# Kernel optimization log

Measured on AMD Instinct MI355X. Metric: run time of the kernel, lower is better.

The kernel has to match this reference:

```python
import jax, jax.numpy as jnp
import numpy as np

WINDOW_SIZES = (1, 2, 3)
COV_DIM = 128
MEM_DIM = 128
BATCH = 8192


def setup_inputs() -> dict:
    rng = np.random.default_rng(0)
    sizes = rng.integers(16, 64, size=BATCH)
    total = int(sizes.sum())  # ~327k tokens
    key = jax.random.key(0)
    ks = jax.random.split(key, 10)
    s = 0.05
    inp = {
        "x": jax.random.normal(ks[0], (total, COV_DIM), jnp.float32),
        "sizes": jnp.asarray(sizes, jnp.int32),
    }
    for i, w in enumerate(WINDOW_SIZES):
        inp[f"conv_w{i}"] = jax.random.normal(ks[1 + 2 * i], (MEM_DIM, COV_DIM, w), jnp.float32) * s
        inp[f"conv_b{i}"] = jax.random.normal(ks[2 + 2 * i], (MEM_DIM,), jnp.float32) * s
    inp["lin_w"] = jax.random.normal(ks[7], (MEM_DIM, len(WINDOW_SIZES) * MEM_DIM), jnp.float32) * s
    inp["lin_b"] = jax.random.normal(ks[8], (MEM_DIM,), jnp.float32) * s
    return inp


def _temporal_conv(x, w, b):
    # x: [T, C], w: [M, C, k] -> [T-k+1, M]  (valid 1D conv, as nn.Conv1d)
    y = jax.lax.conv_general_dilated(
        x.T[None],  # [1, C, T]
        w,
        window_strides=(1,),
        padding="VALID",
        dimension_numbers=("NCH", "OIH", "NCH"),
    )[0]  # [M, L]
    return y.T + b


def _dmax(h, sizes, window_size, batch):
    # Ragged per-segment max over dim 0 of the concatenated conv output.
    # Segment i covers rows [off_i, off_i + sizes[i] - window_size + 1) where
    # off_i is the exclusive cumsum of sizes (DMax advances start_idx by sizes[i]).
    L = h.shape[0]  # total - window_size + 1
    cum = jnp.cumsum(sizes)  # [B], inclusive
    p = jnp.arange(L)
    seg = jnp.searchsorted(cum, p, side="right")  # segment owning row p
    valid = p + (window_size - 1) < cum[seg]  # within sizes[i]-w+1 prefix
    seg = jnp.where(valid, seg, batch)  # dump invalid rows in a trash segment
    return jax.ops.segment_max(h, seg, num_segments=batch + 1)[:batch]


def reference(x, sizes, conv_w0, conv_b0, conv_w1, conv_b1, conv_w2, conv_b2, lin_w, lin_b):
    batch = sizes.shape[0]
    convs = ((conv_w0, conv_b0), (conv_w1, conv_b1), (conv_w2, conv_b2))
    pools = []
    for wsz, (cw, cb) in zip(WINDOW_SIZES, convs):
        h = jax.nn.relu(_temporal_conv(x, cw, cb))  # [T-w+1, M]
        pools.append(_dmax(h, sizes, wsz, batch))  # [B, M]
    concat = jnp.concatenate(pools, axis=1)  # [B, 3M]
    return jnp.tanh(concat @ lin_w.T + lin_b)  # [B, M]
```

## Files before the change

kernel.cpp:

```cpp
#include <hip/hip_runtime.h>
#include <hip/hip_bf16.h>

typedef __bf16 bf16x8 __attribute__((ext_vector_type(8)));
typedef __bf16 bf16x4 __attribute__((ext_vector_type(4)));
typedef float  f32x4  __attribute__((ext_vector_type(4)));

#define MFMA16(a, b, c) __builtin_amdgcn_mfma_f32_16x16x32_bf16((a), (b), (c), 0, 0, 0)

__global__ void k_prep(const int* __restrict__ sizes, int* __restrict__ offsets,
                       const float* __restrict__ w0, const float* __restrict__ w1,
                       const float* __restrict__ w2, const float* __restrict__ lw,
                       __bf16* __restrict__ Wpack,
                       __bf16* __restrict__ Lhi, __bf16* __restrict__ Llo) {
  const int bid = blockIdx.x, t = threadIdx.x;
  if (bid == 240) {
    __shared__ int part[256];
    const int base = t * 32;
    int v[32];
    int s = 0;
#pragma unroll
    for (int i = 0; i < 32; ++i) { v[i] = sizes[base + i]; s += v[i]; }
    part[t] = s;
    __syncthreads();
    for (int d = 1; d < 256; d <<= 1) {
      int add = (t >= d) ? part[t - d] : 0;
      __syncthreads();
      part[t] += add;
      __syncthreads();
    }
    int run = (t == 0) ? 0 : part[t - 1];
#pragma unroll
    for (int i = 0; i < 32; ++i) { offsets[base + i] = run; run += v[i]; }
  } else if (bid < 48) {
    const int nt = bid, sl = nt >> 3, f = nt & 7;
    const int kt = t >> 6, lane = t & 63;
    const float* src; int kw, jj;
    if      (sl == 0) { src = w0; kw = 1; jj = 0; }
    else if (sl == 1) { src = w1; kw = 2; jj = 0; }
    else if (sl == 2) { src = w1; kw = 2; jj = 1; }
    else if (sl == 3) { src = w2; kw = 3; jj = 0; }
    else if (sl == 4) { src = w2; kw = 3; jj = 1; }
    else              { src = w2; kw = 3; jj = 2; }
    const int feat  = f * 16 + (lane & 15);
    const int cbase = kt * 32 + ((lane >> 4) << 3);
    __bf16* dst = Wpack + ((((nt * 4 + kt) << 6) + lane) << 3);
#pragma unroll
    for (int j = 0; j < 8; ++j)
      dst[j] = (__bf16)src[(feat * 128 + cbase + j) * kw + jj];
  } else {
    const int idx = (bid - 48) * 256 + t;
    const int j = idx & 7, lane = (idx >> 3) & 63, rest = idx >> 9;
    const int kt = rest % 12, nt = rest / 12;
    const int o = nt * 16 + (lane & 15);
    const int q = kt * 32 + ((lane >> 4) << 3) + j;
    const float v = lw[o * 384 + q];
    const __bf16 hi = (__bf16)v;
    Lhi[idx] = hi;
    Llo[idx] = (__bf16)(v - (float)hi);
  }
}

__global__ __launch_bounds__(256, 4)
void k_conv(const float* __restrict__ x, const int* __restrict__ sizes,
            const int* __restrict__ offsets,
            const float* __restrict__ cb0, const float* __restrict__ cb1,
            const float* __restrict__ cb2,
            const bf16x8* __restrict__ Wpack,
            __bf16* __restrict__ Phi, __bf16* __restrict__ Plo) {
  __shared__ __bf16 xh[66 * 136];
  const int b = blockIdx.x;
  const int s = sizes[b];
  const long off = offsets[b];
  const int t = threadIdx.x;
  const int MT = (s + 15) >> 4;

  {
    const int quads = s << 5;
    float4 v[8];
#pragma unroll
    for (int i = 0; i < 8; ++i) {
      const int qi = t + (i << 8);
      if (qi < quads) {
        const int r = qi >> 5, c = (qi & 31) << 2;
        v[i] = *(const float4*)(x + (off + r) * 128 + c);
      }
    }
#pragma unroll
    for (int i = 0; i < 8; ++i) {
      const int qi = t + (i << 8);
      if (qi < quads) {
        const int r = qi >> 5, c = (qi & 31) << 2;
        bf16x4 h; h[0] = (__bf16)v[i].x; h[1] = (__bf16)v[i].y;
                  h[2] = (__bf16)v[i].z; h[3] = (__bf16)v[i].w;
        *(bf16x4*)&xh[r * 136 + c] = h;
      }
    }
    const int zend = MT * 16 + 2;
    const int c = (t & 31) << 2;
    for (int r = s + (t >> 5); r < zend; r += 8)
      *(bf16x4*)&xh[r * 136 + c] =
          bf16x4{(__bf16)0.f, (__bf16)0.f, (__bf16)0.f, (__bf16)0.f};
  }
  __syncthreads();

  const int wid = t >> 6, lane = t & 63;
  const int lo16 = lane & 15, g16 = lane >> 4;

#pragma unroll
  for (int fi = 0; fi < 2; ++fi) {
    const int ft = wid + (fi << 2);
    const int feat = ft * 16 + lo16;

    f32x4 acc[4][3];
#pragma unroll
    for (int mt = 0; mt < 4; ++mt)
#pragma unroll
      for (int p = 0; p < 3; ++p)
        acc[mt][p] = f32x4{0.f, 0.f, 0.f, 0.f};

#pragma unroll
    for (int kt = 0; kt < 4; ++kt) {
      bf16x8 bf[6];
#pragma unroll
      for (int sl = 0; sl < 6; ++sl)
        bf[sl] = Wpack[(((sl * 8 + ft) * 4 + kt) << 6) + lane];
#pragma unroll
      for (int mt = 0; mt < 4; ++mt) {
        if (mt < MT) {
          const __bf16* ap = &xh[(mt * 16 + lo16) * 136 + kt * 32 + (g16 << 3)];
          const bf16x8 A0 = *(const bf16x8*)ap;
          const bf16x8 A1 = *(const bf16x8*)(ap + 136);
          const bf16x8 A2 = *(const bf16x8*)(ap + 272);
          acc[mt][0] = MFMA16(A0, bf[0], acc[mt][0]);
          acc[mt][1] = MFMA16(A0, bf[1], acc[mt][1]);
          acc[mt][1] = MFMA16(A1, bf[2], acc[mt][1]);
          acc[mt][2] = MFMA16(A0, bf[3], acc[mt][2]);
          acc[mt][2] = MFMA16(A1, bf[4], acc[mt][2]);
          acc[mt][2] = MFMA16(A2, bf[5], acc[mt][2]);
        }
      }
    }

    float m1 = -1e30f, m2 = -1e30f, m3 = -1e30f;
#pragma unroll
    for (int mt = 0; mt < 4; ++mt) {
      if (mt >= MT) continue;
#pragma unroll
      for (int v = 0; v < 4; ++v) {
        const int lrow = mt * 16 + g16 * 4 + v;
        if (lrow < s)     m1 = fmaxf(m1, acc[mt][0][v]);
        if (lrow < s - 1) m2 = fmaxf(m2, acc[mt][1][v]);
        if (lrow < s - 2) m3 = fmaxf(m3, acc[mt][2][v]);
      }
    }
    m1 = fmaxf(m1, __shfl_xor(m1, 16)); m1 = fmaxf(m1, __shfl_xor(m1, 32));
    m2 = fmaxf(m2, __shfl_xor(m2, 16)); m2 = fmaxf(m2, __shfl_xor(m2, 32));
    m3 = fmaxf(m3, __shfl_xor(m3, 16)); m3 = fmaxf(m3, __shfl_xor(m3, 32));
    if (g16 == 0) {
      const float p1 = fmaxf(m1 + cb0[feat], 0.f);
      const float p2 = fmaxf(m2 + cb1[feat], 0.f);
      const float p3 = fmaxf(m3 + cb2[feat], 0.f);
      const __bf16 h1 = (__bf16)p1, h2 = (__bf16)p2, h3 = (__bf16)p3;
      const long row = (long)b * 384;
      Phi[row + feat]       = h1;
      Plo[row + feat]       = (__bf16)(p1 - (float)h1);
      Phi[row + 128 + feat] = h2;
      Plo[row + 128 + feat] = (__bf16)(p2 - (float)h2);
      Phi[row + 256 + feat] = h3;
      Plo[row + 256 + feat] = (__bf16)(p3 - (float)h3);
    }
  }
}

__global__ __launch_bounds__(256, 4)
void k_lin(const __bf16* __restrict__ Phi, const __bf16* __restrict__ Plo,
           const bf16x8* __restrict__ Lhi, const bf16x8* __restrict__ Llo,
           const float* __restrict__ lb, float* __restrict__ out) {
  __shared__ __bf16 ph[16 * 392];
  __shared__ __bf16 pl[16 * 392];
  const int blk = blockIdx.x, t = threadIdx.x;
  const long rbase = (long)blk * 16;
#pragma unroll
  for (int i = 0; i < 3; ++i) {
    const int ci = t + (i << 8);
    const int r = ci / 48, cc = ci % 48;
    *(int4*)&ph[r * 392 + (cc << 3)] = *(const int4*)&Phi[(rbase + r) * 384 + (cc << 3)];
    *(int4*)&pl[r * 392 + (cc << 3)] = *(const int4*)&Plo[(rbase + r) * 384 + (cc << 3)];
  }
  __syncthreads();
  const int wid = t >> 6, lane = t & 63;
  const int lo16 = lane & 15, g = lane >> 4;
#pragma unroll
  for (int ni = 0; ni < 2; ++ni) {
    const int nt = wid + (ni << 2);
    f32x4 acc = f32x4{0.f, 0.f, 0.f, 0.f};
#pragma unroll
    for (int kt = 0; kt < 12; ++kt) {
      const bf16x8 bh = Lhi[((nt * 12 + kt) << 6) + lane];
      const bf16x8 bl = Llo[((nt * 12 + kt) << 6) + lane];
      const int aoff = lo16 * 392 + kt * 32 + (g << 3);
      const bf16x8 ah = *(const bf16x8*)&ph[aoff];
      const bf16x8 al = *(const bf16x8*)&pl[aoff];
      acc = MFMA16(ah, bh, acc);
      acc = MFMA16(al, bh, acc);
      acc = MFMA16(ah, bl, acc);
    }
    const int o = nt * 16 + lo16;
    const float bias = lb[o];
#pragma unroll
    for (int v = 0; v < 4; ++v) {
      const int r = g * 4 + v;
      const float val = acc[v] + bias;
      out[(rbase + r) * 128 + o] = 1.f - 2.f / (__expf(2.f * val) + 1.f);
    }
  }
}

extern "C" void kernel_launch(void* const* d_in, const int* in_sizes, int n_in,
                              void* d_out, int out_size, void* d_ws, size_t ws_size,
                              hipStream_t stream) {
  const float* x   = (const float*)d_in[0];
  const int* sizes = (const int*)d_in[1];
  const float* w0  = (const float*)d_in[2];
  const float* cb0 = (const float*)d_in[3];
  const float* w1  = (const float*)d_in[4];
  const float* cb1 = (const float*)d_in[5];
  const float* w2  = (const float*)d_in[6];
  const float* cb2 = (const float*)d_in[7];
  const float* lw  = (const float*)d_in[8];
  const float* lb  = (const float*)d_in[9];

  char* ws = (char*)d_ws;
  size_t o = 0;
  int*    offsets = (int*)ws;                 o += 32768;
  __bf16* Wpack   = (__bf16*)(ws + o);        o += 196608;
  __bf16* Lhi     = (__bf16*)(ws + o);        o += 98304;
  __bf16* Llo     = (__bf16*)(ws + o);        o += 98304;
  __bf16* Phi     = (__bf16*)(ws + o);        o += 8192L * 384 * 2;
  __bf16* Plo     = (__bf16*)(ws + o);        o += 8192L * 384 * 2;

  k_prep<<<241, 256, 0, stream>>>(sizes, offsets, w0, w1, w2, lw, Wpack, Lhi, Llo);
  k_conv<<<8192, 256, 0, stream>>>(x, sizes, offsets, cb0, cb1, cb2,
                                   (const bf16x8*)Wpack, Phi, Plo);
  k_lin<<<512, 256, 0, stream>>>(Phi, Plo, (const bf16x8*)Lhi,
                                 (const bf16x8*)Llo, lb, (float*)d_out);
}
```

Measured before the change: 326.4 us.

## Split conv block across 16 waves with row-half partition and LDS max reduction

Each segment's conv block grows from 256 to 1024 threads. The 16 waves are split into 8 feature tiles by 2 row halves, and each wave computes two M-tiles instead of four across two feature passes. Partial maxima are merged through a small shared array and an extra barrier. Out-of-range rows are masked by seeding the accumulator with -1e30, replacing the per-element compares. The goal is more wave-level parallelism and less work per wave. The cost is extra weight loads from duplicated B fragments, an extra sync, and the launch_bounds(1024,8) register cap, which may cause spills.

```diff
diff --git a/kernel.cpp b/kernel.cpp
--- a/kernel.cpp
+++ b/kernel.cpp
@@ -60,7 +60,7 @@
   }
 }
 
-__global__ __launch_bounds__(256, 4)
+__global__ __launch_bounds__(1024, 8)
 void k_conv(const float* __restrict__ x, const int* __restrict__ sizes,
             const int* __restrict__ offsets,
             const float* __restrict__ cb0, const float* __restrict__ cb1,
@@ -68,6 +68,7 @@
             const bf16x8* __restrict__ Wpack,
             __bf16* __restrict__ Phi, __bf16* __restrict__ Plo) {
   __shared__ __bf16 xh[66 * 136];
+  __shared__ float  part[16 * 48];
   const int b = blockIdx.x;
   const int s = sizes[b];
   const long off = offsets[b];
@@ -76,99 +77,117 @@
 
   {
     const int quads = s << 5;
-    float4 v[8];
-#pragma unroll
-    for (int i = 0; i < 8; ++i) {
-      const int qi = t + (i << 8);
-      if (qi < quads) {
-        const int r = qi >> 5, c = (qi & 31) << 2;
-        v[i] = *(const float4*)(x + (off + r) * 128 + c);
-      }
-    }
-#pragma unroll
-    for (int i = 0; i < 8; ++i) {
-      const int qi = t + (i << 8);
-      if (qi < quads) {
-        const int r = qi >> 5, c = (qi & 31) << 2;
-        bf16x4 h; h[0] = (__bf16)v[i].x; h[1] = (__bf16)v[i].y;
-                  h[2] = (__bf16)v[i].z; h[3] = (__bf16)v[i].w;
-        *(bf16x4*)&xh[r * 136 + c] = h;
-      }
+    float4 v0, v1;
+    const bool p0 = t < quads, p1 = t + 1024 < quads;
+    if (p0) {
+      const int r = t >> 5, c = (t & 31) << 2;
+      v0 = *(const float4*)(x + (off + r) * 128 + c);
+    }
+    if (p1) {
+      const int qi = t + 1024;
+      const int r = qi >> 5, c = (qi & 31) << 2;
+      v1 = *(const float4*)(x + (off + r) * 128 + c);
+    }
+    if (p0) {
+      const int r = t >> 5, c = (t & 31) << 2;
+      bf16x4 h; h[0] = (__bf16)v0.x; h[1] = (__bf16)v0.y;
+                h[2] = (__bf16)v0.z; h[3] = (__bf16)v0.w;
+      *(bf16x4*)&xh[r * 136 + c] = h;
+    }
+    if (p1) {
+      const int qi = t + 1024;
+      const int r = qi >> 5, c = (qi & 31) << 2;
+      bf16x4 h; h[0] = (__bf16)v1.x; h[1] = (__bf16)v1.y;
+                h[2] = (__bf16)v1.z; h[3] = (__bf16)v1.w;
+      *(bf16x4*)&xh[r * 136 + c] = h;
     }
     const int zend = MT * 16 + 2;
-    const int c = (t & 31) << 2;
-    for (int r = s + (t >> 5); r < zend; r += 8)
+    const int r = s + (t >> 5), c = (t & 31) << 2;
+    if (r < zend)
       *(bf16x4*)&xh[r * 136 + c] =
           bf16x4{(__bf16)0.f, (__bf16)0.f, (__bf16)0.f, (__bf16)0.f};
   }
   __syncthreads();
 
   const int wid = t >> 6, lane = t & 63;
+  const int ft = wid & 7, mh = wid >> 3;
   const int lo16 = lane & 15, g16 = lane >> 4;
-
-#pragma unroll
-  for (int fi = 0; fi < 2; ++fi) {
-    const int ft = wid + (fi << 2);
-    const int feat = ft * 16 + lo16;
-
-    f32x4 acc[4][3];
-#pragma unroll
-    for (int mt = 0; mt < 4; ++mt)
-#pragma unroll
-      for (int p = 0; p < 3; ++p)
-        acc[mt][p] = f32x4{0.f, 0.f, 0.f, 0.f};
-
+  const int mt0 = mh << 1;
+
+  f32x4 acc[2][3];
+#pragma unroll
+  for (int am = 0; am < 2; ++am)
+#pragma unroll
+    for (int p = 0; p < 3; ++p)
+#pragma unroll
+      for (int v = 0; v < 4; ++v) {
+        const int lrow = (mt0 + am) * 16 + g16 * 4 + v;
+        acc[am][p][v] = (lrow < s - p) ? 0.f : -1e30f;
+      }
+
+  if (mt0 < MT) {
 #pragma unroll
     for (int kt = 0; kt < 4; ++kt) {
-      bf16x8 bf[6];
-#pragma unroll
-      for (int sl = 0; sl < 6; ++sl)
-        bf[sl] = Wpack[(((sl * 8 + ft) * 4 + kt) << 6) + lane];
-#pragma unroll
-      for (int mt = 0; mt < 4; ++mt) {
+      const int bbase = ((ft * 4 + kt) << 6) + lane;
+      const bf16x8 bf0 = Wpack[bbase];
+      const bf16x8 bf1 = Wpack[bbase + (8 * 4 << 6)];
+      const bf16x8 bf2 = Wpack[bbase + (16 * 4 << 6)];
+      const bf16x8 bf3 = Wpack[bbase + (24 * 4 << 6)];
+      const bf16x8 bf4 = Wpack[bbase + (32 * 4 << 6)];
+      const bf16x8 bf5 = Wpack[bbase + (40 * 4 << 6)];
+#pragma unroll
+      for (int am = 0; am < 2; ++am) {
+        const int mt = mt0 + am;
         if (mt < MT) {
           const __bf16* ap = &xh[(mt * 16 + lo16) * 136 + kt * 32 + (g16 << 3)];
-          const bf16x8 A0 = *(const bf16x8*)ap;
-          const bf16x8 A1 = *(const bf16x8*)(ap + 136);
-          const bf16x8 A2 = *(const bf16x8*)(ap + 272);
-          acc[mt][0] = MFMA16(A0, bf[0], acc[mt][0]);
-          acc[mt][1] = MFMA16(A0, bf[1], acc[mt][1]);
-          acc[mt][1] = MFMA16(A1, bf[2], acc[mt][1]);
-          acc[mt][2] = MFMA16(A0, bf[3], acc[mt][2]);
-          acc[mt][2] = MFMA16(A1, bf[4], acc[mt][2]);
-          acc[mt][2] = MFMA16(A2, bf[5], acc[mt][2]);
+          bf16x8 A = *(const bf16x8*)ap;
+          acc[am][0] = MFMA16(A, bf0, acc[am][0]);
+          acc[am][1] = MFMA16(A, bf1, acc[am][1]);
+          acc[am][2] = MFMA16(A, bf3, acc[am][2]);
+          A = *(const bf16x8*)(ap + 136);
+          acc[am][1] = MFMA16(A, bf2, acc[am][1]);
+          acc[am][2] = MFMA16(A, bf4, acc[am][2]);
+          A = *(const bf16x8*)(ap + 272);
+          acc[am][2] = MFMA16(A, bf5, acc[am][2]);
         }
       }
     }
-
-    float m1 = -1e30f, m2 = -1e30f, m3 = -1e30f;
-#pragma unroll
-    for (int mt = 0; mt < 4; ++mt) {
-      if (mt >= MT) continue;
-#pragma unroll
-      for (int v = 0; v < 4; ++v) {
-        const int lrow = mt * 16 + g16 * 4 + v;
-        if (lrow < s)     m1 = fmaxf(m1, acc[mt][0][v]);
-        if (lrow < s - 1) m2 = fmaxf(m2, acc[mt][1][v]);
-        if (lrow < s - 2) m3 = fmaxf(m3, acc[mt][2][v]);
-      }
-    }
-    m1 = fmaxf(m1, __shfl_xor(m1, 16)); m1 = fmaxf(m1, __shfl_xor(m1, 32));
-    m2 = fmaxf(m2, __shfl_xor(m2, 16)); m2 = fmaxf(m2, __shfl_xor(m2, 32));
-    m3 = fmaxf(m3, __shfl_xor(m3, 16)); m3 = fmaxf(m3, __shfl_xor(m3, 32));
-    if (g16 == 0) {
-      const float p1 = fmaxf(m1 + cb0[feat], 0.f);
-      const float p2 = fmaxf(m2 + cb1[feat], 0.f);
-      const float p3 = fmaxf(m3 + cb2[feat], 0.f);
-      const __bf16 h1 = (__bf16)p1, h2 = (__bf16)p2, h3 = (__bf16)p3;
-      const long row = (long)b * 384;
-      Phi[row + feat]       = h1;
-      Plo[row + feat]       = (__bf16)(p1 - (float)h1);
-      Phi[row + 128 + feat] = h2;
-      Plo[row + 128 + feat] = (__bf16)(p2 - (float)h2);
-      Phi[row + 256 + feat] = h3;
-      Plo[row + 256 + feat] = (__bf16)(p3 - (float)h3);
-    }
+  }
+
+  float m[3];
+#pragma unroll
+  for (int p = 0; p < 3; ++p) {
+    float mm = acc[0][p][0];
+#pragma unroll
+    for (int v = 1; v < 4; ++v) mm = fmaxf(mm, acc[0][p][v]);
+#pragma unroll
+    for (int v = 0; v < 4; ++v) mm = fmaxf(mm, acc[1][p][v]);
+    mm = fmaxf(mm, __shfl_xor(mm, 16));
+    mm = fmaxf(mm, __shfl_xor(mm, 32));
+    m[p] = mm;
+  }
+  if (g16 == 0) {
+    part[wid * 48 + lo16]      = m[0];
+    part[wid * 48 + 16 + lo16] = m[1];
+    part[wid * 48 + 32 + lo16] = m[2];
+  }
+  __syncthreads();
+  if (mh == 0 && g16 == 0) {
+    const int feat = ft * 16 + lo16;
+    const float m1 = fmaxf(part[wid * 48 + lo16],      part[(wid + 8) * 48 + lo16]);
+    const float m2 = fmaxf(part[wid * 48 + 16 + lo16], part[(wid + 8) * 48 + 16 + lo16]);
+    const float m3 = fmaxf(part[wid * 48 + 32 + lo16], part[(wid + 8) * 48 + 32 + lo16]);
+    const float p1 = fmaxf(m1 + cb0[feat], 0.f);
+    const float p2 = fmaxf(m2 + cb1[feat], 0.f);
+    const float p3 = fmaxf(m3 + cb2[feat], 0.f);
+    const __bf16 h1 = (__bf16)p1, h2 = (__bf16)p2, h3 = (__bf16)p3;
+    const long row = (long)b * 384;
+    Phi[row + feat]       = h1;
+    Plo[row + feat]       = (__bf16)(p1 - (float)h1);
+    Phi[row + 128 + feat] = h2;
+    Plo[row + 128 + feat] = (__bf16)(p2 - (float)h2);
+    Phi[row + 256 + feat] = h3;
+    Plo[row + 256 + feat] = (__bf16)(p3 - (float)h3);
   }
 }
 
@@ -240,8 +259,8 @@
   __bf16* Plo     = (__bf16*)(ws + o);        o += 8192L * 384 * 2;
 
   k_prep<<<241, 256, 0, stream>>>(sizes, offsets, w0, w1, w2, lw, Wpack, Lhi, Llo);
-  k_conv<<<8192, 256, 0, stream>>>(x, sizes, offsets, cb0, cb1, cb2,
-                                   (const bf16x8*)Wpack, Phi, Plo);
+  k_conv<<<8192, 1024, 0, stream>>>(x, sizes, offsets, cb0, cb1, cb2,
+                                    (const bf16x8*)Wpack, Phi, Plo);
   k_lin<<<512, 256, 0, stream>>>(Phi, Plo, (const bf16x8*)Lhi,
                                  (const bf16x8*)Llo, lb, (float*)d_out);
 }
```

After: 341.3 us. 4.5% more time.

## Pre-convert x to bf16 and double-buffer segments via direct global-to-LDS loads

Applied to the files above, without the earlier changes.

A pass added to the prep kernel converts the whole fp32 input to bf16 in workspace. The conv kernel then handles 8 segments per block and double-buffers them in LDS with global_load_lds, using an XOR-swizzled layout so the next segment's fetch overlaps the current segment's MFMAs. Row masking moves into the accumulator initialisation (-1e30 for invalid rows), which simplifies the max reduction. The cost is an extra full read and write of x in bf16, and tails are handled by clamping loads to the last row and relying on the init-time masking.

```diff
diff --git a/kernel.cpp b/kernel.cpp
--- a/kernel.cpp
+++ b/kernel.cpp
@@ -7,13 +7,28 @@
 
 #define MFMA16(a, b, c) __builtin_amdgcn_mfma_f32_16x16x32_bf16((a), (b), (c), 0, 0, 0)
 
+#define GLD_LDS16(g, l) \
+  __builtin_amdgcn_global_load_lds((const __attribute__((address_space(1))) void*)(g), \
+                                   (__attribute__((address_space(3))) void*)(l), 16, 0, 0)
+
 __global__ void k_prep(const int* __restrict__ sizes, int* __restrict__ offsets,
                        const float* __restrict__ w0, const float* __restrict__ w1,
                        const float* __restrict__ w2, const float* __restrict__ lw,
+                       const float* __restrict__ x, __bf16* __restrict__ xb, int nx,
                        __bf16* __restrict__ Wpack,
                        __bf16* __restrict__ Lhi, __bf16* __restrict__ Llo) {
   const int bid = blockIdx.x, t = threadIdx.x;
-  if (bid == 240) {
+  if (bid >= 241) {
+    const int n4 = nx >> 2;
+    int i = (bid - 241) * 256 + t;
+    const int stride = (gridDim.x - 241) * 256;
+    for (; i < n4; i += stride) {
+      const float4 v = *(const float4*)(x + (size_t)i * 4);
+      bf16x4 h; h[0] = (__bf16)v.x; h[1] = (__bf16)v.y;
+                h[2] = (__bf16)v.z; h[3] = (__bf16)v.w;
+      *(bf16x4*)&xb[(size_t)i * 4] = h;
+    }
+  } else if (bid == 240) {
     __shared__ int part[256];
     const int base = t * 32;
     int v[32];
@@ -61,113 +76,125 @@
 }
 
 __global__ __launch_bounds__(256, 4)
-void k_conv(const float* __restrict__ x, const int* __restrict__ sizes,
-            const int* __restrict__ offsets,
+void k_conv(const __bf16* __restrict__ xb, const int* __restrict__ sizes,
+            const int* __restrict__ offsets, int Tm1,
             const float* __restrict__ cb0, const float* __restrict__ cb1,
             const float* __restrict__ cb2,
             const bf16x8* __restrict__ Wpack,
             __bf16* __restrict__ Phi, __bf16* __restrict__ Plo) {
-  __shared__ __bf16 xh[66 * 136];
-  const int b = blockIdx.x;
-  const int s = sizes[b];
-  const long off = offsets[b];
+  __shared__ __bf16 xs[2 * 66 * 128];
   const int t = threadIdx.x;
-  const int MT = (s + 15) >> 4;
-
-  {
-    const int quads = s << 5;
-    float4 v[8];
-#pragma unroll
-    for (int i = 0; i < 8; ++i) {
-      const int qi = t + (i << 8);
-      if (qi < quads) {
-        const int r = qi >> 5, c = (qi & 31) << 2;
-        v[i] = *(const float4*)(x + (off + r) * 128 + c);
-      }
-    }
-#pragma unroll
-    for (int i = 0; i < 8; ++i) {
-      const int qi = t + (i << 8);
-      if (qi < quads) {
-        const int r = qi >> 5, c = (qi & 31) << 2;
-        bf16x4 h; h[0] = (__bf16)v[i].x; h[1] = (__bf16)v[i].y;
-                  h[2] = (__bf16)v[i].z; h[3] = (__bf16)v[i].w;
-        *(bf16x4*)&xh[r * 136 + c] = h;
-      }
-    }
-    const int zend = MT * 16 + 2;
-    const int c = (t & 31) << 2;
-    for (int r = s + (t >> 5); r < zend; r += 8)
-      *(bf16x4*)&xh[r * 136 + c] =
-          bf16x4{(__bf16)0.f, (__bf16)0.f, (__bf16)0.f, (__bf16)0.f};
-  }
-  __syncthreads();
-
   const int wid = t >> 6, lane = t & 63;
   const int lo16 = lane & 15, g16 = lane >> 4;
-
-#pragma unroll
-  for (int fi = 0; fi < 2; ++fi) {
-    const int ft = wid + (fi << 2);
-    const int feat = ft * 16 + lo16;
-
-    f32x4 acc[4][3];
-#pragma unroll
-    for (int mt = 0; mt < 4; ++mt)
-#pragma unroll
-      for (int p = 0; p < 3; ++p)
-        acc[mt][p] = f32x4{0.f, 0.f, 0.f, 0.f};
-
-#pragma unroll
-    for (int kt = 0; kt < 4; ++kt) {
-      bf16x8 bf[6];
-#pragma unroll
-      for (int sl = 0; sl < 6; ++sl)
-        bf[sl] = Wpack[(((sl * 8 + ft) * 4 + kt) << 6) + lane];
-#pragma unroll
-      for (int mt = 0; mt < 4; ++mt) {
-        if (mt < MT) {
-          const __bf16* ap = &xh[(mt * 16 + lo16) * 136 + kt * 32 + (g16 << 3)];
-          const bf16x8 A0 = *(const bf16x8*)ap;
-          const bf16x8 A1 = *(const bf16x8*)(ap + 136);
-          const bf16x8 A2 = *(const bf16x8*)(ap + 272);
-          acc[mt][0] = MFMA16(A0, bf[0], acc[mt][0]);
-          acc[mt][1] = MFMA16(A0, bf[1], acc[mt][1]);
-          acc[mt][1] = MFMA16(A1, bf[2], acc[mt][1]);
-          acc[mt][2] = MFMA16(A0, bf[3], acc[mt][2]);
-          acc[mt][2] = MFMA16(A1, bf[4], acc[mt][2]);
-          acc[mt][2] = MFMA16(A2, bf[5], acc[mt][2]);
+  const int b0 = blockIdx.x << 3;
+
+  if (t < 64) {
+    const int buf = t >> 5, row = 64 + ((t >> 4) & 1), sl = t & 15;
+    *(bf16x8*)&xs[buf * 8448 + row * 128 + sl * 8] =
+        bf16x8{(__bf16)0.f,(__bf16)0.f,(__bf16)0.f,(__bf16)0.f,
+               (__bf16)0.f,(__bf16)0.f,(__bf16)0.f,(__bf16)0.f};
+  }
+
+  int aoff[3][4];
+#pragma unroll
+  for (int tap = 0; tap < 3; ++tap) {
+    const int rr = lo16 + tap;
+#pragma unroll
+    for (int kt = 0; kt < 4; ++kt)
+      aoff[tap][kt] = rr * 256 + ((((kt << 2) + g16) ^ (rr & 7)) << 4);
+  }
+  const char* xsb = (const char*)xs;
+
+  auto stage = [&](int off_n, int bufsel) {
+    __bf16* lb = &xs[bufsel * 8448];
+    const int rl = lane >> 4, cl = lane & 15;
+#pragma unroll
+    for (int i = 0; i < 4; ++i) {
+      const int q = (wid << 2) + i;
+      const int r = (q << 2) + rl;
+      const int grow = min(off_n + r, Tm1);
+      const __bf16* src = xb + (size_t)grow * 128 + ((cl ^ (r & 7)) << 3);
+      GLD_LDS16(src, lb + q * 512);
+    }
+  };
+
+  stage(offsets[b0], 0);
+
+  for (int g = 0; g < 8; ++g) {
+    const int bufoff = (g & 1) * 16896;
+    __syncthreads();
+    if (g < 7) stage(offsets[b0 + g + 1], (g + 1) & 1);
+
+    const int b = b0 + g;
+    const int s = sizes[b];
+    const int MT = (s + 15) >> 4;
+
+#pragma unroll
+    for (int fi = 0; fi < 2; ++fi) {
+      const int ft = wid + (fi << 2);
+      const int feat = ft * 16 + lo16;
+
+      f32x4 acc[4][3];
+#pragma unroll
+      for (int mt = 0; mt < 4; ++mt)
+#pragma unroll
+        for (int p = 0; p < 3; ++p)
+#pragma unroll
+          for (int v = 0; v < 4; ++v)
+            acc[mt][p][v] = (mt * 16 + g16 * 4 + v < s - p) ? 0.f : -1e30f;
+
+#pragma unroll
+      for (int kt = 0; kt < 4; ++kt) {
+        const int bbase = ((ft * 4 + kt) << 6) + lane;
+        const bf16x8 bf0 = Wpack[bbase];
+        const bf16x8 bf1 = Wpack[bbase + 2048];
+        const bf16x8 bf2 = Wpack[bbase + 4096];
+        const bf16x8 bf3 = Wpack[bbase + 6144];
+        const bf16x8 bf4 = Wpack[bbase + 8192];
+        const bf16x8 bf5 = Wpack[bbase + 10240];
+#pragma unroll
+        for (int mt = 0; mt < 4; ++mt) {
+          if (mt < MT) {
+            const int ab = bufoff + mt * 4096;
+            const bf16x8 A0 = *(const bf16x8*)(xsb + ab + aoff[0][kt]);
+            const bf16x8 A1 = *(const bf16x8*)(xsb + ab + aoff[1][kt]);
+            const bf16x8 A2 = *(const bf16x8*)(xsb + ab + aoff[2][kt]);
+            acc[mt][0] = MFMA16(A0, bf0, acc[mt][0]);
+            acc[mt][1] = MFMA16(A0, bf1, acc[mt][1]);
+            acc[mt][1] = MFMA16(A1, bf2, acc[mt][1]);
+            acc[mt][2] = MFMA16(A0, bf3, acc[mt][2]);
+            acc[mt][2] = MFMA16(A1, bf4, acc[mt][2]);
+            acc[mt][2] = MFMA16(A2, bf5, acc[mt][2]);
+          }
         }
       }
-    }
-
-    float m1 = -1e30f, m2 = -1e30f, m3 = -1e30f;
-#pragma unroll
-    for (int mt = 0; mt < 4; ++mt) {
-      if (mt >= MT) continue;
-#pragma unroll
-      for (int v = 0; v < 4; ++v) {
-        const int lrow = mt * 16 + g16 * 4 + v;
-        if (lrow < s)     m1 = fmaxf(m1, acc[mt][0][v]);
-        if (lrow < s - 1) m2 = fmaxf(m2, acc[mt][1][v]);
-        if (lrow < s - 2) m3 = fmaxf(m3, acc[mt][2][v]);
+
+      float m[3];
+#pragma unroll
+      for (int p = 0; p < 3; ++p) {
+        float mm = fmaxf(fmaxf(acc[0][p][0], acc[0][p][1]),
+                         fmaxf(acc[0][p][2], acc[0][p][3]));
+#pragma unroll
+        for (int mt = 1; mt < 4; ++mt)
+          mm = fmaxf(mm, fmaxf(fmaxf(acc[mt][p][0], acc[mt][p][1]),
+                               fmaxf(acc[mt][p][2], acc[mt][p][3])));
+        mm = fmaxf(mm, __shfl_xor(mm, 16));
+        mm = fmaxf(mm, __shfl_xor(mm, 32));
+        m[p] = mm;
       }
-    }
-    m1 = fmaxf(m1, __shfl_xor(m1, 16)); m1 = fmaxf(m1, __shfl_xor(m1, 32));
-    m2 = fmaxf(m2, __shfl_xor(m2, 16)); m2 = fmaxf(m2, __shfl_xor(m2, 32));
-    m3 = fmaxf(m3, __shfl_xor(m3, 16)); m3 = fmaxf(m3, __shfl_xor(m3, 32));
-    if (g16 == 0) {
-      const float p1 = fmaxf(m1 + cb0[feat], 0.f);
-      const float p2 = fmaxf(m2 + cb1[feat], 0.f);
-      const float p3 = fmaxf(m3 + cb2[feat], 0.f);
-      const __bf16 h1 = (__bf16)p1, h2 = (__bf16)p2, h3 = (__bf16)p3;
-      const long row = (long)b * 384;
-      Phi[row + feat]       = h1;
-      Plo[row + feat]       = (__bf16)(p1 - (float)h1);
-      Phi[row + 128 + feat] = h2;
-      Plo[row + 128 + feat] = (__bf16)(p2 - (float)h2);
-      Phi[row + 256 + feat] = h3;
-      Plo[row + 256 + feat] = (__bf16)(p3 - (float)h3);
+      if (g16 == 0) {
+        const float p1 = fmaxf(m[0] + cb0[feat], 0.f);
+        const float p2 = fmaxf(m[1] + cb1[feat], 0.f);
+        const float p3 = fmaxf(m[2] + cb2[feat], 0.f);
+        const __bf16 h1 = (__bf16)p1, h2 = (__bf16)p2, h3 = (__bf16)p3;
+        const long row = (long)b * 384;
+        Phi[row + feat]       = h1;
+        Plo[row + feat]       = (__bf16)(p1 - (float)h1);
+        Phi[row + 128 + feat] = h2;
+        Plo[row + 128 + feat] = (__bf16)(p2 - (float)h2);
+        Phi[row + 256 + feat] = h3;
+        Plo[row + 256 + feat] = (__bf16)(p3 - (float)h3);
+      }
     }
   }
 }
@@ -230,6 +257,9 @@
   const float* lw  = (const float*)d_in[8];
   const float* lb  = (const float*)d_in[9];
 
+  const int nx = in_sizes[0];
+  const int T  = nx / 128;
+
   char* ws = (char*)d_ws;
   size_t o = 0;
   int*    offsets = (int*)ws;                 o += 32768;
@@ -238,10 +268,12 @@
   __bf16* Llo     = (__bf16*)(ws + o);        o += 98304;
   __bf16* Phi     = (__bf16*)(ws + o);        o += 8192L * 384 * 2;
   __bf16* Plo     = (__bf16*)(ws + o);        o += 8192L * 384 * 2;
-
-  k_prep<<<241, 256, 0, stream>>>(sizes, offsets, w0, w1, w2, lw, Wpack, Lhi, Llo);
-  k_conv<<<8192, 256, 0, stream>>>(x, sizes, offsets, cb0, cb1, cb2,
-                                   (const bf16x8*)Wpack, Phi, Plo);
+  __bf16* xbuf    = (__bf16*)(ws + o);        o += (size_t)nx * 2;
+
+  k_prep<<<2048, 256, 0, stream>>>(sizes, offsets, w0, w1, w2, lw,
+                                   x, xbuf, nx, Wpack, Lhi, Llo);
+  k_conv<<<1024, 256, 0, stream>>>(xbuf, sizes, offsets, T - 1,
+                                   cb0, cb1, cb2, (const bf16x8*)Wpack, Phi, Plo);
   k_lin<<<512, 256, 0, stream>>>(Phi, Plo, (const bf16x8*)Lhi,
                                  (const bf16x8*)Llo, lb, (float*)d_out);
 }
```

Result: slower. 961.0 us (+194.4%).
